# Optimization experiments

Measured on AMD Instinct MI355X. Metric: run time of the kernel, lower is better.

The kernel has to match this reference:

```python
import jax, jax.numpy as jnp
import numpy as np

GRID_SIZE = 16
KH = KW = 3


def setup_inputs() -> dict:
    key = jax.random.key(0)
    k1, k2, k3, k4 = jax.random.split(key, 4)
    B, H, W, C, F = 8, 32, 32, 64, 64
    x = jax.random.normal(k1, (B, H, W, C), dtype=jnp.float32)
    control_points = jax.random.normal(k2, (F, C, KH, KW, GRID_SIZE), dtype=jnp.float32) * 0.1
    w1 = jax.random.normal(k3, (F, C, KH, KW), dtype=jnp.float32) * 0.1
    w2 = jax.random.normal(k4, (F, C, KH, KW), dtype=jnp.float32) * 0.1
    return {"x": x, "control_points": control_points, "w1": w1, "w2": w2}


def _extract_patches_same(x, kh, kw):
    # x: (B,H,W,C), stride 1, TF 'SAME' padding -> (B,H,W,kh,kw,C)
    B, H, W, C = x.shape
    ph, pw = kh - 1, kw - 1
    xp = jnp.pad(x, ((0, 0), (ph // 2, ph - ph // 2), (pw // 2, pw - pw // 2), (0, 0)))
    taps = [xp[:, i:i + H, j:j + W, :] for i in range(kh) for j in range(kw)]
    return jnp.stack(taps, axis=3).reshape(B, H, W, kh, kw, C)


def reference(x, control_points, w1, w2):
    F, C, kh, kw, G = control_points.shape
    grid = jnp.linspace(-1.0, 1.0, G)
    patches = _extract_patches_same(x, kh, kw)  # (B,H,W,kh,kw,C)
    # spline: searchsorted + clip + linear interp on the fixed uniform grid
    xc = jnp.clip(patches, -1.0, 1.0)
    idx = jnp.clip(jnp.searchsorted(grid, xc, side='left') - 1, 0, G - 2)
    frac = (xc - grid[idx]) / (grid[idx + 1] - grid[idx])  # (B,H,W,kh,kw,C)
    # two-nonzero linear basis over control points -> (B,H,W,kh,kw,C,G)
    basis = (jax.nn.one_hot(idx, G, dtype=x.dtype) * (1.0 - frac)[..., None]
             + jax.nn.one_hot(idx + 1, G, dtype=x.dtype) * frac[..., None])
    # fuse w1 into control points, contract taps+channels+grid in one einsum
    wcp = w1[..., None] * control_points  # (F,C,kh,kw,G)
    out = jnp.einsum('bpqijcg,fcijg->bpqf', basis, wcp)
    out = out + jnp.einsum('bpqijc,fcij->bpqf', jax.nn.silu(patches), w2)
    return out  # (B,H,W,F)
```

## Files before the change

### kernel.cpp

```cpp
#include <hip/hip_runtime.h>


typedef _Float16 v8h __attribute__((ext_vector_type(8)));
typedef float    v4f __attribute__((ext_vector_type(4)));

#define NSLOT   655360
#define PARTOFF 1310720
#define NPART   524288

__global__ __launch_bounds__(256) void prep_wsw(const float* __restrict__ cp,
                                                const float* __restrict__ w1,
                                                const float* __restrict__ w2,
                                                _Float16* __restrict__ wsw) {
    int tid  = blockIdx.x * 256 + threadIdx.x;
    int j    = tid & 7;
    int lane = (tid >> 3) & 63;
    int rest = tid >> 9;
    int nt   = rest & 3;
    int ks   = rest >> 2;
    int k    = ks * 32 + ((lane >> 4) << 3) + j;
    int f    = (nt << 4) + (lane & 15);
    int chunk = k / 640;
    int kl    = k - chunk * 640;
    float val = 0.f;
    if (kl < 576) {
        int c = (chunk << 2) + kl / 144;
        int r = kl % 144;
        val = w1[f * 576 + c * 9 + (r >> 4)] * cp[f * 9216 + c * 144 + r];
    } else {
        int i2 = kl - 576;
        int ij = i2 & 15;
        if (ij < 9) {
            int c = (chunk << 2) + (i2 >> 4);
            val = w2[f * 576 + c * 9 + ij];
        }
    }
    wsw[tid] = (_Float16)val;
}

__global__ __launch_bounds__(256, 3) void kan_mfma(const float* __restrict__ x,
                                                   const _Float16* __restrict__ wsw,
                                                   float* __restrict__ part) {
    __shared__ __align__(16) char smem[41472];
    _Float16* sb  = (_Float16*)smem;
    float*    red = (float*)smem;

    int blk   = blockIdx.x;
    int kh    = blk >> 8;
    int rowid = blk & 255;
    int b = rowid >> 5, p = rowid & 31;
    int t = threadIdx.x, wv = t >> 6, lane = t & 63;
    int m = lane & 15, kq = lane >> 4;

    const int chs[4] = {0, 6, 11, 16};
    int ch0 = chs[kh], ch1 = chs[kh + 1];

    v4f z4 = (v4f){0.f, 0.f, 0.f, 0.f};
    for (int i4 = t; i4 < 2592; i4 += 256) ((v4f*)sb)[i4] = z4;

    const float* xb = x + (size_t)b * 65536;
    int  off0[5], sbb[5], sil[5];
    bool okv[5];
#pragma unroll
    for (int it = 0; it < 5; ++it) {
        int e  = t + it * 256;
        int ec = e < 1152 ? e : 0;
        int px = ec / 36;
        int r  = ec - px * 36;
        int cl = r / 9;
        int ij = r - cl * 9;
        int di = ij / 3;
        int dj = ij - di * 3;
        int row = p + di - 1;
        int col = px + dj - 1;
        okv[it]  = ((unsigned)row < 32u) && ((unsigned)col < 32u) && (e < 1152);
        off0[it] = okv[it] ? ((row * 32 + col) * 64 + cl) : 0;
        sbb[it]  = px * 648 + cl * 144 + ij * 16;
        sil[it]  = px * 648 + 576 + cl * 16 + ij;
    }

    v4f acc[2][4];
#pragma unroll
    for (int i = 0; i < 2; ++i)
#pragma unroll
        for (int n = 0; n < 4; ++n) acc[i][n] = z4;

    float vbuf[5];
#pragma unroll
    for (int it = 0; it < 5; ++it)
        vbuf[it] = okv[it] ? xb[off0[it] + ch0 * 4] : 0.f;

    int prevIdx[5];
    __syncthreads();

    for (int gch = ch0; gch < ch1; ++gch) {
#pragma unroll
        for (int it = 0; it < 5; ++it) {
            if (t + it * 256 < 1152) {
                float v  = vbuf[it];
                float xc = fminf(fmaxf(v, -1.f), 1.f);
                float tt = (xc + 1.f) * 7.5f;
                int idx  = (int)tt;
                if (idx > 14) idx = 14;
                float fr = tt - (float)idx;
                float sv = v * __builtin_amdgcn_rcpf(1.f + __expf(-v));
                _Float16* rowp = sb + sbb[it];
                if (gch > ch0) {
                    int pi = prevIdx[it];
                    rowp[pi]     = (_Float16)0.f;
                    rowp[pi + 1] = (_Float16)0.f;
                }
                rowp[idx]     = (_Float16)(1.f - fr);
                rowp[idx + 1] = (_Float16)fr;
                sb[sil[it]]   = (_Float16)sv;
                prevIdx[it] = idx;
            }
        }
        if (gch + 1 < ch1) {
#pragma unroll
            for (int it = 0; it < 5; ++it)
                vbuf[it] = okv[it] ? xb[off0[it] + (gch + 1) * 4] : 0.f;
        }
        __syncthreads();
        const _Float16* ap0 = sb + m * 648 + (wv * 5) * 32 + kq * 8;
        const v8h* bp = (const v8h*)wsw + ((size_t)gch * 20 + wv * 5) * 256 + lane;
#pragma unroll
        for (int s = 0; s < 5; ++s) {
            v8h a0 = *(const v8h*)(ap0 + s * 32);
            v8h a1 = *(const v8h*)(ap0 + s * 32 + 16 * 648);
            v8h b0 = bp[s * 256];
            v8h b1 = bp[s * 256 + 64];
            v8h b2 = bp[s * 256 + 128];
            v8h b3 = bp[s * 256 + 192];
            acc[0][0] = __builtin_amdgcn_mfma_f32_16x16x32_f16(a0, b0, acc[0][0], 0, 0, 0);
            acc[0][1] = __builtin_amdgcn_mfma_f32_16x16x32_f16(a0, b1, acc[0][1], 0, 0, 0);
            acc[0][2] = __builtin_amdgcn_mfma_f32_16x16x32_f16(a0, b2, acc[0][2], 0, 0, 0);
            acc[0][3] = __builtin_amdgcn_mfma_f32_16x16x32_f16(a0, b3, acc[0][3], 0, 0, 0);
            acc[1][0] = __builtin_amdgcn_mfma_f32_16x16x32_f16(a1, b0, acc[1][0], 0, 0, 0);
            acc[1][1] = __builtin_amdgcn_mfma_f32_16x16x32_f16(a1, b1, acc[1][1], 0, 0, 0);
            acc[1][2] = __builtin_amdgcn_mfma_f32_16x16x32_f16(a1, b2, acc[1][2], 0, 0, 0);
            acc[1][3] = __builtin_amdgcn_mfma_f32_16x16x32_f16(a1, b3, acc[1][3], 0, 0, 0);
        }
        __syncthreads();
    }

#pragma unroll
    for (int mt = 0; mt < 2; ++mt)
#pragma unroll
        for (int nt = 0; nt < 4; ++nt)
#pragma unroll
            for (int r = 0; r < 4; ++r)
                red[wv * 2080 + (mt * 16 + kq * 4 + r) * 65 + nt * 16 + m] = acc[mt][nt][r];
    __syncthreads();
    int f = t & 63, pxg = t >> 6;
    float* op = part + (size_t)kh * NPART + rowid * 2048 + f;
#pragma unroll
    for (int i = 0; i < 8; ++i) {
        int px = pxg * 8 + i;
        float s = red[px * 65 + f] + red[2080 + px * 65 + f]
                + red[4160 + px * 65 + f] + red[6240 + px * 65 + f];
        op[px * 64] = s;
    }
}

__global__ __launch_bounds__(256) void combine(const float* __restrict__ part,
                                               float* __restrict__ out) {
    int i = blockIdx.x * 256 + threadIdx.x;
    v4f a = ((const v4f*)part)[i];
    v4f b = ((const v4f*)(part + NPART))[i];
    v4f c = ((const v4f*)(part + 2 * NPART))[i];
    ((v4f*)out)[i] = a + b + c;
}

extern "C" void kernel_launch(void* const* d_in, const int* in_sizes, int n_in,
                              void* d_out, int out_size, void* d_ws, size_t ws_size,
                              hipStream_t stream) {
    const float* x  = (const float*)d_in[0];
    const float* cp = (const float*)d_in[1];
    const float* w1 = (const float*)d_in[2];
    const float* w2 = (const float*)d_in[3];
    _Float16* wsw = (_Float16*)d_ws;
    float*    prt = (float*)((char*)d_ws + PARTOFF);

    prep_wsw<<<NSLOT / 256, 256, 0, stream>>>(cp, w1, w2, wsw);
    kan_mfma<<<768, 256, 0, stream>>>(x, wsw, prt);
    combine<<<512, 256, 0, stream>>>(prt, (float*)d_out);
}
```

Before: 90.47 us.

## Vectorize weight prep, load x as float4 per patch, software-pipeline MFMA operand loads

The weight-prep kernel now has each thread build a full 8-wide half vector from vectorized control-point loads, which cuts its launch from 2560 to 320 blocks. In the main kernel, each thread handles one (pixel, tap) pair and loads four channels at once as a float4. The previous spline indices are packed into one register, which lowers per-thread register and address state. The MFMA loop double-buffers its A and B fragment loads so the next step's loads overlap the current step's MFMAs. The next x prefetch is moved after the barrier, and the LDS zeroing is placed after the first x load.

```diff
diff --git a/kernel.cpp b/kernel.cpp
--- a/kernel.cpp
+++ b/kernel.cpp
@@ -13,29 +13,41 @@
                                                 const float* __restrict__ w2,
                                                 _Float16* __restrict__ wsw) {
     int tid  = blockIdx.x * 256 + threadIdx.x;
-    int j    = tid & 7;
-    int lane = (tid >> 3) & 63;
-    int rest = tid >> 9;
+    int lane = tid & 63;
+    int rest = tid >> 6;
     int nt   = rest & 3;
     int ks   = rest >> 2;
-    int k    = ks * 32 + ((lane >> 4) << 3) + j;
+    int kb   = ks * 32 + ((lane >> 4) << 3);
     int f    = (nt << 4) + (lane & 15);
-    int chunk = k / 640;
-    int kl    = k - chunk * 640;
-    float val = 0.f;
-    if (kl < 576) {
-        int c = (chunk << 2) + kl / 144;
-        int r = kl % 144;
-        val = w1[f * 576 + c * 9 + (r >> 4)] * cp[f * 9216 + c * 144 + r];
+    int chunk = kb / 640;
+    int klb   = kb - chunk * 640;
+    v8h out;
+    if (klb < 576) {
+        int c  = (chunk << 2) + klb / 144;
+        int rb = klb % 144;
+        int ij = rb >> 4;
+        float w = w1[f * 576 + c * 9 + ij];
+        const v4f* cpp = (const v4f*)(cp + (size_t)f * 9216 + c * 144 + rb);
+        v4f lo = cpp[0], hi = cpp[1];
+#pragma unroll
+        for (int j = 0; j < 4; ++j) {
+            out[j]     = (_Float16)(w * lo[j]);
+            out[j + 4] = (_Float16)(w * hi[j]);
+        }
     } else {
-        int i2 = kl - 576;
-        int ij = i2 & 15;
-        if (ij < 9) {
-            int c = (chunk << 2) + (i2 >> 4);
-            val = w2[f * 576 + c * 9 + ij];
-        }
-    }
-    wsw[tid] = (_Float16)val;
+        int i2 = klb - 576;
+        int c  = (chunk << 2) + (i2 >> 4);
+        if ((i2 & 15) == 0) {
+#pragma unroll
+            for (int j = 0; j < 8; ++j)
+                out[j] = (_Float16)w2[f * 576 + c * 9 + j];
+        } else {
+#pragma unroll
+            for (int j = 0; j < 8; ++j) out[j] = (_Float16)0.f;
+            out[0] = (_Float16)w2[f * 576 + c * 9 + 8];
+        }
+    }
+    ((v8h*)wsw)[tid] = out;
 }
 
 __global__ __launch_bounds__(256, 3) void kan_mfma(const float* __restrict__ x,
@@ -55,29 +67,34 @@
     const int chs[4] = {0, 6, 11, 16};
     int ch0 = chs[kh], ch1 = chs[kh + 1];
 
-    v4f z4 = (v4f){0.f, 0.f, 0.f, 0.f};
-    for (int i4 = t; i4 < 2592; i4 += 256) ((v4f*)sb)[i4] = z4;
-
     const float* xb = x + (size_t)b * 65536;
-    int  off0[5], sbb[5], sil[5];
-    bool okv[5];
-#pragma unroll
-    for (int it = 0; it < 5; ++it) {
+
+    int xoff[2], sbb[2], silb[2];
+    unsigned prevPack[2] = {0u, 0u};
+#pragma unroll
+    for (int it = 0; it < 2; ++it) {
         int e  = t + it * 256;
-        int ec = e < 1152 ? e : 0;
-        int px = ec / 36;
-        int r  = ec - px * 36;
-        int cl = r / 9;
-        int ij = r - cl * 9;
+        int ec = e < 288 ? e : 0;
+        int px = ec / 9;
+        int ij = ec - px * 9;
         int di = ij / 3;
         int dj = ij - di * 3;
         int row = p + di - 1;
         int col = px + dj - 1;
-        okv[it]  = ((unsigned)row < 32u) && ((unsigned)col < 32u) && (e < 1152);
-        off0[it] = okv[it] ? ((row * 32 + col) * 64 + cl) : 0;
-        sbb[it]  = px * 648 + cl * 144 + ij * 16;
-        sil[it]  = px * 648 + 576 + cl * 16 + ij;
-    }
+        bool ok  = ((unsigned)row < 32u) && ((unsigned)col < 32u);
+        xoff[it] = ok ? ((row * 32 + col) * 64) : -1;
+        sbb[it]  = px * 648 + ij * 16;
+        silb[it] = px * 648 + 576 + ij;
+    }
+
+    v4f z4 = (v4f){0.f, 0.f, 0.f, 0.f};
+
+    v4f vbuf[2];
+#pragma unroll
+    for (int it = 0; it < 2; ++it)
+        vbuf[it] = (xoff[it] >= 0) ? *(const v4f*)(xb + xoff[it] + ch0 * 4) : z4;
+
+    for (int i4 = t; i4 < 2592; i4 += 256) ((v4f*)sb)[i4] = z4;
 
     v4f acc[2][4];
 #pragma unroll
@@ -85,61 +102,77 @@
 #pragma unroll
         for (int n = 0; n < 4; ++n) acc[i][n] = z4;
 
-    float vbuf[5];
-#pragma unroll
-    for (int it = 0; it < 5; ++it)
-        vbuf[it] = okv[it] ? xb[off0[it] + ch0 * 4] : 0.f;
-
-    int prevIdx[5];
     __syncthreads();
 
     for (int gch = ch0; gch < ch1; ++gch) {
 #pragma unroll
-        for (int it = 0; it < 5; ++it) {
-            if (t + it * 256 < 1152) {
-                float v  = vbuf[it];
-                float xc = fminf(fmaxf(v, -1.f), 1.f);
-                float tt = (xc + 1.f) * 7.5f;
-                int idx  = (int)tt;
-                if (idx > 14) idx = 14;
-                float fr = tt - (float)idx;
-                float sv = v * __builtin_amdgcn_rcpf(1.f + __expf(-v));
-                _Float16* rowp = sb + sbb[it];
-                if (gch > ch0) {
-                    int pi = prevIdx[it];
-                    rowp[pi]     = (_Float16)0.f;
-                    rowp[pi + 1] = (_Float16)0.f;
+        for (int it = 0; it < 2; ++it) {
+            if (t + it * 256 < 288) {
+                v4f xv = vbuf[it];
+                unsigned pp = prevPack[it];
+                unsigned np = 0;
+                _Float16* rp = sb + sbb[it];
+                _Float16* sp = sb + silb[it];
+#pragma unroll
+                for (int cl = 0; cl < 4; ++cl) {
+                    float v  = xv[cl];
+                    float xc = fminf(fmaxf(v, -1.f), 1.f);
+                    float tt = (xc + 1.f) * 7.5f;
+                    int idx  = (int)tt;
+                    if (idx > 14) idx = 14;
+                    float fr = tt - (float)idx;
+                    float sv = v * __builtin_amdgcn_rcpf(1.f + __expf(-v));
+                    _Float16* q = rp + cl * 144;
+                    if (gch > ch0) {
+                        int pi = (pp >> (cl * 8)) & 255;
+                        q[pi]     = (_Float16)0.f;
+                        q[pi + 1] = (_Float16)0.f;
+                    }
+                    q[idx]     = (_Float16)(1.f - fr);
+                    q[idx + 1] = (_Float16)fr;
+                    sp[cl * 16] = (_Float16)sv;
+                    np |= (unsigned)idx << (cl * 8);
                 }
-                rowp[idx]     = (_Float16)(1.f - fr);
-                rowp[idx + 1] = (_Float16)fr;
-                sb[sil[it]]   = (_Float16)sv;
-                prevIdx[it] = idx;
+                prevPack[it] = np;
             }
         }
+        __syncthreads();
         if (gch + 1 < ch1) {
 #pragma unroll
-            for (int it = 0; it < 5; ++it)
-                vbuf[it] = okv[it] ? xb[off0[it] + (gch + 1) * 4] : 0.f;
-        }
-        __syncthreads();
-        const _Float16* ap0 = sb + m * 648 + (wv * 5) * 32 + kq * 8;
+            for (int it = 0; it < 2; ++it)
+                vbuf[it] = (xoff[it] >= 0)
+                         ? *(const v4f*)(xb + xoff[it] + (gch + 1) * 4) : z4;
+        }
+        const _Float16* ap = sb + m * 648 + (wv * 5) * 32 + kq * 8;
         const v8h* bp = (const v8h*)wsw + ((size_t)gch * 20 + wv * 5) * 256 + lane;
+        v8h a0c = *(const v8h*)ap;
+        v8h a1c = *(const v8h*)(ap + 16 * 648);
+        v8h b0c = bp[0], b1c = bp[64], b2c = bp[128], b3c = bp[192];
 #pragma unroll
         for (int s = 0; s < 5; ++s) {
-            v8h a0 = *(const v8h*)(ap0 + s * 32);
-            v8h a1 = *(const v8h*)(ap0 + s * 32 + 16 * 648);
-            v8h b0 = bp[s * 256];
-            v8h b1 = bp[s * 256 + 64];
-            v8h b2 = bp[s * 256 + 128];
-            v8h b3 = bp[s * 256 + 192];
-            acc[0][0] = __builtin_amdgcn_mfma_f32_16x16x32_f16(a0, b0, acc[0][0], 0, 0, 0);
-            acc[0][1] = __builtin_amdgcn_mfma_f32_16x16x32_f16(a0, b1, acc[0][1], 0, 0, 0);
-            acc[0][2] = __builtin_amdgcn_mfma_f32_16x16x32_f16(a0, b2, acc[0][2], 0, 0, 0);
-            acc[0][3] = __builtin_amdgcn_mfma_f32_16x16x32_f16(a0, b3, acc[0][3], 0, 0, 0);
-            acc[1][0] = __builtin_amdgcn_mfma_f32_16x16x32_f16(a1, b0, acc[1][0], 0, 0, 0);
-            acc[1][1] = __builtin_amdgcn_mfma_f32_16x16x32_f16(a1, b1, acc[1][1], 0, 0, 0);
-            acc[1][2] = __builtin_amdgcn_mfma_f32_16x16x32_f16(a1, b2, acc[1][2], 0, 0, 0);
-            acc[1][3] = __builtin_amdgcn_mfma_f32_16x16x32_f16(a1, b3, acc[1][3], 0, 0, 0);
+            v8h a0n, a1n, b0n, b1n, b2n, b3n;
+            if (s < 4) {
+                const _Float16* ap2 = ap + (s + 1) * 32;
+                a0n = *(const v8h*)ap2;
+                a1n = *(const v8h*)(ap2 + 16 * 648);
+                const v8h* bp2 = bp + (s + 1) * 256;
+                b0n = bp2[0];
+                b1n = bp2[64];
+                b2n = bp2[128];
+                b3n = bp2[192];
+            }
+            acc[0][0] = __builtin_amdgcn_mfma_f32_16x16x32_f16(a0c, b0c, acc[0][0], 0, 0, 0);
+            acc[0][1] = __builtin_amdgcn_mfma_f32_16x16x32_f16(a0c, b1c, acc[0][1], 0, 0, 0);
+            acc[0][2] = __builtin_amdgcn_mfma_f32_16x16x32_f16(a0c, b2c, acc[0][2], 0, 0, 0);
+            acc[0][3] = __builtin_amdgcn_mfma_f32_16x16x32_f16(a0c, b3c, acc[0][3], 0, 0, 0);
+            acc[1][0] = __builtin_amdgcn_mfma_f32_16x16x32_f16(a1c, b0c, acc[1][0], 0, 0, 0);
+            acc[1][1] = __builtin_amdgcn_mfma_f32_16x16x32_f16(a1c, b1c, acc[1][1], 0, 0, 0);
+            acc[1][2] = __builtin_amdgcn_mfma_f32_16x16x32_f16(a1c, b2c, acc[1][2], 0, 0, 0);
+            acc[1][3] = __builtin_amdgcn_mfma_f32_16x16x32_f16(a1c, b3c, acc[1][3], 0, 0, 0);
+            if (s < 4) {
+                a0c = a0n; a1c = a1n;
+                b0c = b0n; b1c = b1n; b2c = b2n; b3c = b3n;
+            }
         }
         __syncthreads();
     }
@@ -182,7 +215,7 @@
     _Float16* wsw = (_Float16*)d_ws;
     float*    prt = (float*)((char*)d_ws + PARTOFF);
 
-    prep_wsw<<<NSLOT / 256, 256, 0, stream>>>(cp, w1, w2, wsw);
+    prep_wsw<<<320, 256, 0, stream>>>(cp, w1, w2, wsw);
     kan_mfma<<<768, 256, 0, stream>>>(x, wsw, prt);
     combine<<<512, 256, 0, stream>>>(prt, (float*)d_out);
 }
```

Result: no change. 90.21 us (-0.3%).
